# Kernel tuning notes

Measured on AMD Instinct MI355X. Metric: run time of the kernel, lower is better.

## Reference

```python
import jax, jax.numpy as jnp
import numpy as np

NPOINT = 1024
RADIUS = 0.2
NSAMPLE = 32
EPS = 1e-5


def farthest_point_sample(xyz, npoint):
    # xyz: [B, N, 3] -> [B, npoint] int32, deterministic start at index 0
    B, N, _ = xyz.shape

    def step(carry, _):
        dist, farthest = carry
        centroid = jnp.take_along_axis(xyz, farthest[:, None, None], axis=1)  # [B,1,3]
        d = jnp.sum((xyz - centroid) ** 2, axis=-1)  # [B,N]
        dist = jnp.minimum(dist, d)
        nxt = jnp.argmax(dist, axis=-1).astype(jnp.int32)
        return (dist, nxt), farthest

    init = (jnp.full((B, N), 1e10, dtype=xyz.dtype), jnp.zeros((B,), dtype=jnp.int32))
    _, idxs = jax.lax.scan(step, init, None, length=npoint)
    return idxs.T  # [B, npoint]


def query_ball_point(radius, nsample, xyz, new_xyz):
    # xyz: [B,N,3], new_xyz: [B,S,3] -> [B,S,nsample] int32
    N = xyz.shape[1]
    sqr = jnp.sum((new_xyz[:, :, None, :] - xyz[:, None, :, :]) ** 2, axis=-1)  # [B,S,N]
    ar = jnp.arange(N, dtype=jnp.int32)
    gidx = jnp.where(sqr > radius ** 2, N, ar[None, None, :])
    gidx = jnp.sort(gidx, axis=-1)[:, :, :nsample]  # sorts index values, matching torch
    first = gidx[:, :, :1]
    return jnp.where(gidx == N, first, gidx)


def mlp_layer(h, w, b, g, be, m, v):
    # h: [B, Cin, K, S]; 1x1 Conv2d + BatchNorm2d(eval) + ReLU
    h = jnp.einsum('oc,bcks->boks', w, h) + b[None, :, None, None]
    h = (h - m[None, :, None, None]) * (g[None, :, None, None] / jnp.sqrt(v[None, :, None, None] + EPS)) + be[None, :, None, None]
    return jax.nn.relu(h)


def setup_inputs() -> dict:
    key = jax.random.key(0)
    ks = jax.random.split(key, 24)
    inp = {
        'xyz': jax.random.normal(ks[0], (1, 16, 3, 4096), jnp.float32),
        'points': jax.random.normal(ks[1], (1, 16, 64, 4096), jnp.float32),
        'w0': jax.random.normal(ks[2], (64, 67), jnp.float32) * 0.1,
        'b0': jax.random.normal(ks[3], (64,), jnp.float32) * 0.1,
        'g0': jax.random.uniform(ks[4], (64,), jnp.float32),
        'be0': jax.random.normal(ks[5], (64,), jnp.float32) * 0.1,
        'm0': jax.random.normal(ks[6], (64,), jnp.float32) * 0.1,
        'v0': jax.random.uniform(ks[7], (64,), jnp.float32),
        'w1': jax.random.normal(ks[8], (64, 64), jnp.float32) * 0.1,
        'b1': jax.random.normal(ks[9], (64,), jnp.float32) * 0.1,
        'g1': jax.random.uniform(ks[10], (64,), jnp.float32),
        'be1': jax.random.normal(ks[11], (64,), jnp.float32) * 0.1,
        'm1': jax.random.normal(ks[12], (64,), jnp.float32) * 0.1,
        'v1': jax.random.uniform(ks[13], (64,), jnp.float32),
        'w2': jax.random.normal(ks[14], (128, 64), jnp.float32) * 0.1,
        'b2': jax.random.normal(ks[15], (128,), jnp.float32) * 0.1,
        'g2': jax.random.uniform(ks[16], (128,), jnp.float32),
        'be2': jax.random.normal(ks[17], (128,), jnp.float32) * 0.1,
        'm2': jax.random.normal(ks[18], (128,), jnp.float32) * 0.1,
        'v2': jax.random.uniform(ks[19], (128,), jnp.float32),
    }
    return inp


def reference(xyz, points, w0, b0, g0, be0, m0, v0, w1, b1, g1, be1, m1, v1, w2, b2, g2, be2, m2, v2):
    T, B, C, N = xyz.shape
    BT = T * B
    x = xyz.reshape(BT, C, N).transpose(0, 2, 1)          # [B', N, 3]
    p = points.reshape(BT, -1, N).transpose(0, 2, 1)      # [B', N, D]

    fps_idx = farthest_point_sample(x, NPOINT)            # [B', S]
    bidx = jnp.arange(BT)[:, None]
    new_xyz = x[bidx, fps_idx]                            # [B', S, 3]

    idx = query_ball_point(RADIUS, NSAMPLE, x, new_xyz)   # [B', S, K]
    b3 = jnp.arange(BT)[:, None, None]
    grouped_xyz = x[b3, idx]                              # [B', S, K, 3]
    grouped_norm = grouped_xyz - new_xyz[:, :, None, :]
    grouped_p = p[b3, idx]                                # [B', S, K, D]
    new_points = jnp.concatenate([grouped_norm, grouped_p], axis=-1)  # [B', S, K, 3+D]

    h = new_points.transpose(0, 3, 2, 1)                  # [B', 3+D, K, S]
    h = mlp_layer(h, w0, b0, g0, be0, m0, v0)
    h = mlp_layer(h, w1, b1, g1, be1, m1, v1)
    h = mlp_layer(h, w2, b2, g2, be2, m2, v2)
    out = jnp.max(h, axis=2)                              # [B', Cout, S]

    new_xyz_out = new_xyz.transpose(0, 2, 1).reshape(T, B, C, NPOINT)
    return new_xyz_out, out
```

## Files before the change

### kernel.cpp

```cpp
#include <hip/hip_runtime.h>
#include <hip/hip_bf16.h>

#define NPTS    4096
#define NBATCH  16
#define NPOINT  1024
#define NSAMPLE 32

#define ROW_SHR1  0x111
#define ROW_SHR2  0x112
#define ROW_SHR4  0x114
#define ROW_SHR8  0x118
#define ROW_BC15  0x142
#define ROW_BC31  0x143

template<int CTRL>
__device__ __forceinline__ unsigned dpp_mov(unsigned v) {
    return (unsigned)__builtin_amdgcn_update_dpp(0, (int)v, CTRL, 0xF, 0xF, true);
}
template<int CTRL>
__device__ __forceinline__ unsigned long long dpp_max64(unsigned long long k) {
    unsigned lo = dpp_mov<CTRL>((unsigned)(k & 0xFFFFFFFFull));
    unsigned hi = dpp_mov<CTRL>((unsigned)(k >> 32));
    unsigned long long t = ((unsigned long long)hi << 32) | (unsigned long long)lo;
    return (t > k) ? t : k;
}
template<int CTRL>
__device__ __forceinline__ float dpp_maxf(float v) {
    unsigned t = dpp_mov<CTRL>(__float_as_uint(v));
    return fmaxf(v, __uint_as_float(t));
}

__global__ __launch_bounds__(512) void fps_kernel(
    const float* __restrict__ xyz, float* __restrict__ newxyz)
{
    const int b    = blockIdx.x;
    const int tid  = threadIdx.x;
    const int lane = tid & 63;
    const int w    = tid >> 6;
    const float* xb = xyz + (size_t)b * 3 * NPTS;

    __shared__ float X[NPTS], Y[NPTS], Z[NPTS];
    __shared__ unsigned long long slots[2][8];

    float px[8], py[8], pz[8], dist[8];
    #pragma unroll
    for (int j = 0; j < 8; ++j) {
        int n = tid + j * 512;
        px[j] = xb[n]; py[j] = xb[NPTS + n]; pz[j] = xb[2*NPTS + n];
        X[n] = px[j];  Y[n] = py[j];         Z[n] = pz[j];
        dist[j] = 1e10f;
    }
    __syncthreads();

    int f = 0;
    if (tid == 0) {
        newxyz[b*3*NPOINT + 0]        = X[0];
        newxyz[b*3*NPOINT + NPOINT]   = Y[0];
        newxyz[b*3*NPOINT + 2*NPOINT] = Z[0];
    }

    for (int i = 1; i < NPOINT; ++i) {
        const float cx = X[f], cy = Y[f], cz = Z[f];
        float bv = -1.0f; int bi = 0;
        #pragma unroll
        for (int j = 0; j < 8; ++j) {
            float dx = px[j] - cx;
            float dy = py[j] - cy;
            float dz = pz[j] - cz;
            float d = __fadd_rn(__fadd_rn(__fmul_rn(dx,dx), __fmul_rn(dy,dy)),
                                __fmul_rn(dz,dz));
            float nd = fminf(dist[j], d);
            dist[j] = nd;
            if (nd > bv) { bv = nd; bi = tid + j*512; }
        }
        unsigned long long key =
            ((unsigned long long)__float_as_uint(bv) << 32) |
            (unsigned long long)(unsigned)(~bi);
        key = dpp_max64<ROW_SHR1>(key);
        key = dpp_max64<ROW_SHR2>(key);
        key = dpp_max64<ROW_SHR4>(key);
        key = dpp_max64<ROW_SHR8>(key);
        key = dpp_max64<ROW_BC15>(key);
        key = dpp_max64<ROW_BC31>(key);
        unsigned rlo = (unsigned)__builtin_amdgcn_readlane((int)(unsigned)(key & 0xFFFFFFFFull), 63);
        unsigned rhi = (unsigned)__builtin_amdgcn_readlane((int)(unsigned)(key >> 32), 63);
        if (lane == 0)
            slots[i & 1][w] = ((unsigned long long)rhi << 32) | (unsigned long long)rlo;
        __syncthreads();
        unsigned long long kk = slots[i & 1][lane & 7];
        kk = dpp_max64<ROW_SHR1>(kk);
        kk = dpp_max64<ROW_SHR2>(kk);
        kk = dpp_max64<ROW_SHR4>(kk);
        unsigned flo = (unsigned)__builtin_amdgcn_readlane((int)(unsigned)(kk & 0xFFFFFFFFull), 7);
        f = (int)(~flo);
        if (tid == 0) {
            newxyz[b*3*NPOINT + i]            = X[f];
            newxyz[b*3*NPOINT + NPOINT + i]   = Y[f];
            newxyz[b*3*NPOINT + 2*NPOINT + i] = Z[f];
        }
    }
}

__global__ __launch_bounds__(256) void ball_kernel(
    const float* __restrict__ xyz, const float* __restrict__ newxyz,
    int* __restrict__ ball_idx)
{
    const int gid  = blockIdx.x * 256 + threadIdx.x;
    const int wid  = gid >> 6;
    const int lane = threadIdx.x & 63;
    const int b    = wid >> 10;
    const int m    = wid & (NPOINT - 1);
    const float r2 = (float)(0.2 * 0.2);

    const float* xb = xyz + (size_t)b * 3 * NPTS;
    const float cx = newxyz[b*3*NPOINT + m];
    const float cy = newxyz[b*3*NPOINT + NPOINT + m];
    const float cz = newxyz[b*3*NPOINT + 2*NPOINT + m];
    int* out = ball_idx + (size_t)wid * NSAMPLE;

    int base = 0, first = 0;
    for (int c0 = 0; c0 < NPTS; c0 += 64) {
        const int n = c0 + lane;
        float dx = xb[n] - cx, dy = xb[NPTS+n] - cy, dz = xb[2*NPTS+n] - cz;
        float d = __fadd_rn(__fadd_rn(__fmul_rn(dx,dx), __fmul_rn(dy,dy)),
                            __fmul_rn(dz,dz));
        bool inb = (d <= r2);
        unsigned long long mask = __ballot(inb);
        if (base == 0 && mask != 0ull) first = c0 + (int)__builtin_ctzll(mask);
        int pos = base + __popcll(mask & ((1ull << lane) - 1ull));
        if (inb && pos < NSAMPLE) out[pos] = n;
        base += __popcll(mask);
        if (base >= NSAMPLE) break;
    }
    if (lane < NSAMPLE && lane >= base) out[lane] = first;
}

__global__ __launch_bounds__(256) void setup_kernel(
    const float* __restrict__ w0, const float* __restrict__ b0,
    const float* __restrict__ g0, const float* __restrict__ be0,
    const float* __restrict__ m0, const float* __restrict__ v0,
    const float* __restrict__ w1, const float* __restrict__ b1,
    const float* __restrict__ g1, const float* __restrict__ be1,
    const float* __restrict__ m1, const float* __restrict__ v1,
    const float* __restrict__ b2, const float* __restrict__ g2,
    const float* __restrict__ be2, const float* __restrict__ m2,
    const float* __restrict__ v2, float* __restrict__ wp)
{
    const int t = threadIdx.x;
    for (int i = t; i < 64*67; i += 256) {
        int o = i / 67, k = i - o*67;
        wp[k*64 + o] = w0[i];
    }
    for (int i = t; i < 64*64; i += 256) {
        int o = i >> 6, k = i & 63;
        wp[4288 + k*64 + o] = w1[i];
    }
    if (t < 64) {
        float s0 = g0[t] / sqrtf(v0[t] + 1e-5f);
        wp[8384 + t] = s0;
        wp[8448 + t] = (b0[t] - m0[t]) * s0 + be0[t];
        float s1 = g1[t] / sqrtf(v1[t] + 1e-5f);
        wp[8512 + t] = s1;
        wp[8576 + t] = (b1[t] - m1[t]) * s1 + be1[t];
    }
    if (t < 128) {
        float s2 = g2[t] / sqrtf(v2[t] + 1e-5f);
        wp[8640 + t] = s2;
        wp[8768 + t] = (b2[t] - m2[t]) * s2 + be2[t];
    }
}

__global__ __launch_bounds__(256) void mlp_kernel(
    const float* __restrict__ xyz, const float* __restrict__ points,
    const float* __restrict__ newxyz, const int* __restrict__ ball_idx,
    const float* __restrict__ wp, const float* __restrict__ w2,
    float* __restrict__ out)
{
    const int col = blockIdx.x * 256 + threadIdx.x;
    const int m   = (col >> 5) & (NPOINT - 1);
    const int b   = col >> 15;
    const int p   = ball_idx[col];

    const float* xb = xyz + (size_t)b * 3 * NPTS;
    float in[67];
    in[0] = xb[p]          - newxyz[b*3*NPOINT + m];
    in[1] = xb[NPTS + p]   - newxyz[b*3*NPOINT + NPOINT + m];
    in[2] = xb[2*NPTS + p] - newxyz[b*3*NPOINT + 2*NPOINT + m];
    const float* pb = points + (size_t)b * 64 * NPTS;
    #pragma unroll
    for (int c = 0; c < 64; ++c) in[3 + c] = pb[c * NPTS + p];

    const float* w0t = wp;
    const float* w1t = wp + 4288;
    const float* sc0 = wp + 8384;
    const float* sh0 = wp + 8448;
    const float* sc1 = wp + 8512;
    const float* sh1 = wp + 8576;
    const float* sc2 = wp + 8640;
    const float* sh2 = wp + 8768;

    float h[64];
    #pragma unroll
    for (int o = 0; o < 64; ++o) h[o] = 0.0f;
    #pragma unroll
    for (int k = 0; k < 67; ++k) {
        const float x = in[k];
        #pragma unroll
        for (int o = 0; o < 64; ++o) h[o] = fmaf(w0t[k*64 + o], x, h[o]);
    }
    #pragma unroll
    for (int o = 0; o < 64; ++o)
        h[o] = fmaxf(fmaf(h[o], sc0[o], sh0[o]), 0.0f);

    float g[64];
    #pragma unroll
    for (int o = 0; o < 64; ++o) g[o] = 0.0f;
    #pragma unroll
    for (int k = 0; k < 64; ++k) {
        const float x = h[k];
        #pragma unroll
        for (int o = 0; o < 64; ++o) g[o] = fmaf(w1t[k*64 + o], x, g[o]);
    }
    #pragma unroll
    for (int o = 0; o < 64; ++o)
        g[o] = fmaxf(fmaf(g[o], sc1[o], sh1[o]), 0.0f);

    float* outb = out + (size_t)b * 128 * NPOINT + m;
    #pragma unroll 2
    for (int o = 0; o < 128; ++o) {
        float acc = 0.0f;
        const float* wr = w2 + o * 64;
        #pragma unroll
        for (int k = 0; k < 64; ++k) acc = fmaf(wr[k], g[k], acc);
        acc = fmaxf(fmaf(acc, sc2[o], sh2[o]), 0.0f);
        acc = dpp_maxf<ROW_SHR1>(acc);
        acc = dpp_maxf<ROW_SHR2>(acc);
        acc = dpp_maxf<ROW_SHR4>(acc);
        acc = dpp_maxf<ROW_SHR8>(acc);
        acc = dpp_maxf<ROW_BC15>(acc);
        if ((threadIdx.x & 31) == 31) outb[o * NPOINT] = acc;
    }
}

extern "C" void kernel_launch(void* const* d_in, const int* in_sizes, int n_in,
                              void* d_out, int out_size, void* d_ws, size_t ws_size,
                              hipStream_t stream)
{
    const float* xyz    = (const float*)d_in[0];
    const float* points = (const float*)d_in[1];
    const float* w0  = (const float*)d_in[2];
    const float* b0  = (const float*)d_in[3];
    const float* g0  = (const float*)d_in[4];
    const float* be0 = (const float*)d_in[5];
    const float* m0  = (const float*)d_in[6];
    const float* v0  = (const float*)d_in[7];
    const float* w1  = (const float*)d_in[8];
    const float* b1  = (const float*)d_in[9];
    const float* g1  = (const float*)d_in[10];
    const float* be1 = (const float*)d_in[11];
    const float* m1  = (const float*)d_in[12];
    const float* v1  = (const float*)d_in[13];
    const float* w2  = (const float*)d_in[14];
    const float* b2  = (const float*)d_in[15];
    const float* g2  = (const float*)d_in[16];
    const float* be2 = (const float*)d_in[17];
    const float* m2  = (const float*)d_in[18];
    const float* v2  = (const float*)d_in[19];

    float* out0 = (float*)d_out;
    float* out1 = out0 + NBATCH * 3 * NPOINT;

    int*   ball = (int*)d_ws;
    float* wp   = (float*)((char*)d_ws + (size_t)NBATCH*NPOINT*NSAMPLE*sizeof(int));

    hipLaunchKernelGGL(setup_kernel, dim3(1), dim3(256), 0, stream,
                       w0,b0,g0,be0,m0,v0, w1,b1,g1,be1,m1,v1, b2,g2,be2,m2,v2, wp);
    hipLaunchKernelGGL(fps_kernel,  dim3(NBATCH), dim3(512), 0, stream, xyz, out0);
    hipLaunchKernelGGL(ball_kernel, dim3(NBATCH*NPOINT/4), dim3(256), 0, stream,
                       xyz, out0, ball);
    hipLaunchKernelGGL(mlp_kernel,  dim3(NBATCH*NPOINT*NSAMPLE/256), dim3(256), 0, stream,
                       xyz, points, out0, ball, wp, w2, out1);
}
```

Baseline: 1.173 ms.

## Restructure FPS kernel: fewer waves, float-only wave reduction, packed float4 coords

The FPS kernel now runs with 256 threads per block, each holding 16 contiguous points, which halves the number of waves taking part in each per-iteration barrier and cross-wave reduction. The intra-wave argmax reduces only a 32-bit float through DPP, then recovers the index with a ballot and readlane instead of a 64-bit key reduction. Coordinates are stored in shared memory as float4 so the centroid is fetched with one load. Tie-breaking now follows the lowest lane rather than the lowest global index. Per-thread serial work doubles and register use rises with 16 points per thread.

New measurement: 1.106 ms. 1.06x faster.

```diff
diff --git a/kernel.cpp b/kernel.cpp
--- a/kernel.cpp
+++ b/kernel.cpp
@@ -30,7 +30,7 @@
     return fmaxf(v, __uint_as_float(t));
 }
 
-__global__ __launch_bounds__(512) void fps_kernel(
+__global__ __launch_bounds__(256) void fps_kernel(
     const float* __restrict__ xyz, float* __restrict__ newxyz)
 {
     const int b    = blockIdx.x;
@@ -39,31 +39,40 @@
     const int w    = tid >> 6;
     const float* xb = xyz + (size_t)b * 3 * NPTS;
 
-    __shared__ float X[NPTS], Y[NPTS], Z[NPTS];
-    __shared__ unsigned long long slots[2][8];
-
-    float px[8], py[8], pz[8], dist[8];
-    #pragma unroll
-    for (int j = 0; j < 8; ++j) {
-        int n = tid + j * 512;
-        px[j] = xb[n]; py[j] = xb[NPTS + n]; pz[j] = xb[2*NPTS + n];
-        X[n] = px[j];  Y[n] = py[j];         Z[n] = pz[j];
-        dist[j] = 1e10f;
-    }
+    __shared__ float4 P[NPTS];
+    __shared__ unsigned long long slots[2][4];
+
+    float px[16], py[16], pz[16], dist[16];
+    #pragma unroll
+    for (int q = 0; q < 4; ++q) {
+        const int n4 = tid * 16 + q * 4;
+        float4 xs = *(const float4*)(xb + n4);
+        float4 ys = *(const float4*)(xb + NPTS + n4);
+        float4 zs = *(const float4*)(xb + 2*NPTS + n4);
+        px[q*4+0] = xs.x; px[q*4+1] = xs.y; px[q*4+2] = xs.z; px[q*4+3] = xs.w;
+        py[q*4+0] = ys.x; py[q*4+1] = ys.y; py[q*4+2] = ys.z; py[q*4+3] = ys.w;
+        pz[q*4+0] = zs.x; pz[q*4+1] = zs.y; pz[q*4+2] = zs.z; pz[q*4+3] = zs.w;
+        P[n4+0] = make_float4(xs.x, ys.x, zs.x, 0.f);
+        P[n4+1] = make_float4(xs.y, ys.y, zs.y, 0.f);
+        P[n4+2] = make_float4(xs.z, ys.z, zs.z, 0.f);
+        P[n4+3] = make_float4(xs.w, ys.w, zs.w, 0.f);
+    }
+    #pragma unroll
+    for (int j = 0; j < 16; ++j) dist[j] = 1e10f;
     __syncthreads();
 
-    int f = 0;
+    float4 c0 = P[0];
+    float cx = c0.x, cy = c0.y, cz = c0.z;
     if (tid == 0) {
-        newxyz[b*3*NPOINT + 0]        = X[0];
-        newxyz[b*3*NPOINT + NPOINT]   = Y[0];
-        newxyz[b*3*NPOINT + 2*NPOINT] = Z[0];
+        newxyz[b*3*NPOINT + 0]        = cx;
+        newxyz[b*3*NPOINT + NPOINT]   = cy;
+        newxyz[b*3*NPOINT + 2*NPOINT] = cz;
     }
 
     for (int i = 1; i < NPOINT; ++i) {
-        const float cx = X[f], cy = Y[f], cz = Z[f];
-        float bv = -1.0f; int bi = 0;
+        float bv = -1.0f; int bj = 0;
         #pragma unroll
-        for (int j = 0; j < 8; ++j) {
+        for (int j = 0; j < 16; ++j) {
             float dx = px[j] - cx;
             float dy = py[j] - cy;
             float dz = pz[j] - cz;
@@ -71,32 +80,42 @@
                                 __fmul_rn(dz,dz));
             float nd = fminf(dist[j], d);
             dist[j] = nd;
-            if (nd > bv) { bv = nd; bi = tid + j*512; }
+            if (nd > bv) { bv = nd; bj = j; }
         }
-        unsigned long long key =
-            ((unsigned long long)__float_as_uint(bv) << 32) |
-            (unsigned long long)(unsigned)(~bi);
-        key = dpp_max64<ROW_SHR1>(key);
-        key = dpp_max64<ROW_SHR2>(key);
-        key = dpp_max64<ROW_SHR4>(key);
-        key = dpp_max64<ROW_SHR8>(key);
-        key = dpp_max64<ROW_BC15>(key);
-        key = dpp_max64<ROW_BC31>(key);
-        unsigned rlo = (unsigned)__builtin_amdgcn_readlane((int)(unsigned)(key & 0xFFFFFFFFull), 63);
-        unsigned rhi = (unsigned)__builtin_amdgcn_readlane((int)(unsigned)(key >> 32), 63);
+        const int myidx = (tid << 4) | bj;
+
+        float wv = bv;
+        wv = dpp_maxf<ROW_SHR1>(wv);
+        wv = dpp_maxf<ROW_SHR2>(wv);
+        wv = dpp_maxf<ROW_SHR4>(wv);
+        wv = dpp_maxf<ROW_SHR8>(wv);
+        wv = dpp_maxf<ROW_BC15>(wv);
+        wv = dpp_maxf<ROW_BC31>(wv);
+        float wmax = __uint_as_float(
+            (unsigned)__builtin_amdgcn_readlane((int)__float_as_uint(wv), 63));
+        unsigned long long mask = __ballot(bv == wmax);
+        int L = (int)__builtin_ctzll(mask);
+        int widx = __builtin_amdgcn_readlane(myidx, L);
+
         if (lane == 0)
-            slots[i & 1][w] = ((unsigned long long)rhi << 32) | (unsigned long long)rlo;
+            slots[i & 1][w] =
+                ((unsigned long long)__float_as_uint(wmax) << 32) |
+                (unsigned long long)(unsigned)(~widx);
         __syncthreads();
-        unsigned long long kk = slots[i & 1][lane & 7];
+
+        unsigned long long kk = slots[i & 1][lane & 3];
         kk = dpp_max64<ROW_SHR1>(kk);
         kk = dpp_max64<ROW_SHR2>(kk);
-        kk = dpp_max64<ROW_SHR4>(kk);
-        unsigned flo = (unsigned)__builtin_amdgcn_readlane((int)(unsigned)(kk & 0xFFFFFFFFull), 7);
-        f = (int)(~flo);
+        unsigned flo = (unsigned)__builtin_amdgcn_readlane(
+            (int)(unsigned)(kk & 0xFFFFFFFFull), 3);
+        const int f = (int)(~flo);
+
+        float4 cc = P[f];
+        cx = cc.x; cy = cc.y; cz = cc.z;
         if (tid == 0) {
-            newxyz[b*3*NPOINT + i]            = X[f];
-            newxyz[b*3*NPOINT + NPOINT + i]   = Y[f];
-            newxyz[b*3*NPOINT + 2*NPOINT + i] = Z[f];
+            newxyz[b*3*NPOINT + i]            = cx;
+            newxyz[b*3*NPOINT + NPOINT + i]   = cy;
+            newxyz[b*3*NPOINT + 2*NPOINT + i] = cz;
         }
     }
 }
@@ -275,7 +294,7 @@
 
     hipLaunchKernelGGL(setup_kernel, dim3(1), dim3(256), 0, stream,
                        w0,b0,g0,be0,m0,v0, w1,b1,g1,be1,m1,v1, b2,g2,be2,m2,v2, wp);
-    hipLaunchKernelGGL(fps_kernel,  dim3(NBATCH), dim3(512), 0, stream, xyz, out0);
+    hipLaunchKernelGGL(fps_kernel,  dim3(NBATCH), dim3(256), 0, stream, xyz, out0);
     hipLaunchKernelGGL(ball_kernel, dim3(NBATCH*NPOINT/4), dim3(256), 0, stream,
                        xyz, out0, ball);
     hipLaunchKernelGGL(mlp_kernel,  dim3(NBATCH*NPOINT*NSAMPLE/256), dim3(256), 0, stream,
```

## Restructure FPS kernel to read points from LDS and buffer centroids

Applied to the files above, without the earlier changes.

The farthest-point-sampling kernel no longer keeps each thread's 8 points in registers. It stores coordinates in LDS as interleaved float2 XY plus a separate Z array, filled with vectorized float4 global loads, and reads them back every iteration. The argmax becomes branchless selects on a slot index. Selected centroids go into LDS arrays and are written to global memory in one coalesced pass at the end, instead of tid 0 storing to global each iteration. The aim is to cut register pressure and per-iteration global stores, at the cost of extra LDS loads on the serial critical path of every iteration.

Measured after the change: 1.212 ms. +3.4%, slower.

```diff
diff --git a/kernel.cpp b/kernel.cpp
--- a/kernel.cpp
+++ b/kernel.cpp
@@ -30,7 +30,7 @@
     return fmaxf(v, __uint_as_float(t));
 }
 
-__global__ __launch_bounds__(512) void fps_kernel(
+__global__ __launch_bounds__(512, 1) void fps_kernel(
     const float* __restrict__ xyz, float* __restrict__ newxyz)
 {
     const int b    = blockIdx.x;
@@ -39,65 +39,80 @@
     const int w    = tid >> 6;
     const float* xb = xyz + (size_t)b * 3 * NPTS;
 
-    __shared__ float X[NPTS], Y[NPTS], Z[NPTS];
+    __shared__ float2 XY[NPTS];
+    __shared__ float  Zp[NPTS];
+    __shared__ float  NX[NPOINT], NY[NPOINT], NZ[NPOINT];
     __shared__ unsigned long long slots[2][8];
 
-    float px[8], py[8], pz[8], dist[8];
-    #pragma unroll
-    for (int j = 0; j < 8; ++j) {
-        int n = tid + j * 512;
-        px[j] = xb[n]; py[j] = xb[NPTS + n]; pz[j] = xb[2*NPTS + n];
-        X[n] = px[j];  Y[n] = py[j];         Z[n] = pz[j];
-        dist[j] = 1e10f;
-    }
+    #pragma unroll
+    for (int q = 0; q < 2; ++q) {
+        const int n4 = tid * 8 + q * 4;
+        float4 xs = *(const float4*)(xb + n4);
+        float4 ys = *(const float4*)(xb + NPTS + n4);
+        float4 zs = *(const float4*)(xb + 2*NPTS + n4);
+        XY[n4+0] = make_float2(xs.x, ys.x);  Zp[n4+0] = zs.x;
+        XY[n4+1] = make_float2(xs.y, ys.y);  Zp[n4+1] = zs.y;
+        XY[n4+2] = make_float2(xs.z, ys.z);  Zp[n4+2] = zs.z;
+        XY[n4+3] = make_float2(xs.w, ys.w);  Zp[n4+3] = zs.w;
+    }
+
+    float dist[8];
+    #pragma unroll
+    for (int j = 0; j < 8; ++j) dist[j] = 1e10f;
+
+    float cx = xb[0], cy = xb[NPTS], cz = xb[2*NPTS];
+    if (tid == 0) { NX[0] = cx; NY[0] = cy; NZ[0] = cz; }
     __syncthreads();
 
-    int f = 0;
-    if (tid == 0) {
-        newxyz[b*3*NPOINT + 0]        = X[0];
-        newxyz[b*3*NPOINT + NPOINT]   = Y[0];
-        newxyz[b*3*NPOINT + 2*NPOINT] = Z[0];
-    }
-
     for (int i = 1; i < NPOINT; ++i) {
-        const float cx = X[f], cy = Y[f], cz = Z[f];
-        float bv = -1.0f; int bi = 0;
+        float bv = -1.0f; int bj = 0;
         #pragma unroll
         for (int j = 0; j < 8; ++j) {
-            float dx = px[j] - cx;
-            float dy = py[j] - cy;
-            float dz = pz[j] - cz;
+            float2 xy = XY[j*512 + tid];
+            float  zz = Zp[j*512 + tid];
+            float dx = xy.x - cx;
+            float dy = xy.y - cy;
+            float dz = zz   - cz;
             float d = __fadd_rn(__fadd_rn(__fmul_rn(dx,dx), __fmul_rn(dy,dy)),
                                 __fmul_rn(dz,dz));
             float nd = fminf(dist[j], d);
             dist[j] = nd;
-            if (nd > bv) { bv = nd; bi = tid + j*512; }
+            bool t = nd > bv;
+            bv = t ? nd : bv;
+            bj = t ? j  : bj;
         }
+        const unsigned idx = (unsigned)((bj << 9) + tid);
         unsigned long long key =
             ((unsigned long long)__float_as_uint(bv) << 32) |
-            (unsigned long long)(unsigned)(~bi);
+            (unsigned long long)(unsigned)(~idx);
         key = dpp_max64<ROW_SHR1>(key);
         key = dpp_max64<ROW_SHR2>(key);
         key = dpp_max64<ROW_SHR4>(key);
         key = dpp_max64<ROW_SHR8>(key);
         key = dpp_max64<ROW_BC15>(key);
         key = dpp_max64<ROW_BC31>(key);
-        unsigned rlo = (unsigned)__builtin_amdgcn_readlane((int)(unsigned)(key & 0xFFFFFFFFull), 63);
-        unsigned rhi = (unsigned)__builtin_amdgcn_readlane((int)(unsigned)(key >> 32), 63);
-        if (lane == 0)
-            slots[i & 1][w] = ((unsigned long long)rhi << 32) | (unsigned long long)rlo;
+        if (lane == 63) slots[i & 1][w] = key;
         __syncthreads();
+
         unsigned long long kk = slots[i & 1][lane & 7];
         kk = dpp_max64<ROW_SHR1>(kk);
         kk = dpp_max64<ROW_SHR2>(kk);
         kk = dpp_max64<ROW_SHR4>(kk);
-        unsigned flo = (unsigned)__builtin_amdgcn_readlane((int)(unsigned)(kk & 0xFFFFFFFFull), 7);
-        f = (int)(~flo);
-        if (tid == 0) {
-            newxyz[b*3*NPOINT + i]            = X[f];
-            newxyz[b*3*NPOINT + NPOINT + i]   = Y[f];
-            newxyz[b*3*NPOINT + 2*NPOINT + i] = Z[f];
-        }
+        unsigned flo = (unsigned)__builtin_amdgcn_readlane(
+            (int)(unsigned)(kk & 0xFFFFFFFFull), 7);
+        const int f = (int)(~flo) & (NPTS - 1);
+
+        float2 cxy = XY[f];
+        float  czf = Zp[f];
+        cx = cxy.x; cy = cxy.y; cz = czf;
+        if (tid == 0) { NX[i] = cx; NY[i] = cy; NZ[i] = cz; }
+    }
+
+    __syncthreads();
+    for (int t = tid; t < NPOINT; t += 512) {
+        newxyz[b*3*NPOINT + t]            = NX[t];
+        newxyz[b*3*NPOINT + NPOINT + t]   = NY[t];
+        newxyz[b*3*NPOINT + 2*NPOINT + t] = NZ[t];
     }
 }
 
```
